# Kernel tuning notes

Measured on AMD Instinct MI355X. Metric: run time of the kernel, lower is better.

The kernel has to match this reference:

```python
import jax, jax.numpy as jnp
import numpy as np

EMBED, HIDDEN, VOCAB, FEAT_DIM = 256, 512, 10000, 1024
B, NREG, CAPLEN = 128, 49, 33


def setup_inputs() -> dict:
    key = jax.random.key(0)
    ks = jax.random.split(key, 20)
    xav = lambda k, shp: jax.random.uniform(k, shp, jnp.float32, -1.0, 1.0) * jnp.sqrt(6.0 / (shp[0] + shp[1]))
    d = {
        "features": jax.random.normal(ks[0], (B, NREG, FEAT_DIM), jnp.float32),
        "captions": jax.random.randint(ks[1], (B, CAPLEN), 0, VOCAB),
        "emb": jax.random.uniform(ks[2], (VOCAB, EMBED), jnp.float32, -0.1, 0.1),
        "W_ft": jax.random.uniform(ks[3], (EMBED, FEAT_DIM), jnp.float32, -0.1, 0.1),
        "b_ft": jnp.zeros((EMBED,), jnp.float32),
        "W_i": xav(ks[4], (2 * EMBED, HIDDEN)), "U_i": xav(ks[5], (HIDDEN, HIDDEN)), "b_i": jnp.zeros((HIDDEN,), jnp.float32),
        "W_f": xav(ks[6], (2 * EMBED, HIDDEN)), "U_f": xav(ks[7], (HIDDEN, HIDDEN)), "b_f": jnp.zeros((HIDDEN,), jnp.float32),
        "W_c": xav(ks[8], (2 * EMBED, HIDDEN)), "U_c": xav(ks[9], (HIDDEN, HIDDEN)), "b_c": jnp.zeros((HIDDEN,), jnp.float32),
        "W_o": xav(ks[10], (2 * EMBED, HIDDEN)), "U_o": xav(ks[11], (HIDDEN, HIDDEN)), "b_o": jnp.zeros((HIDDEN,), jnp.float32),
        "W_fc": jax.random.uniform(ks[12], (VOCAB, HIDDEN), jnp.float32, -0.1, 0.1),
        "b_fc": jnp.zeros((VOCAB,), jnp.float32),
    }
    return d


def reference(features, captions, emb, W_ft, b_ft,
              W_i, U_i, b_i, W_f, U_f, b_f, W_c, U_c, b_c, W_o, U_o, b_o,
              W_fc, b_fc):
    # mean-pool image regions, project to embed space
    feats_emb = features.mean(axis=1) @ W_ft.T + b_ft            # [B, E]
    embeds = emb[captions[:, :-1]]                                # [B, T, E]
    xs = jnp.swapaxes(embeds, 0, 1)                               # [T, B, E]

    h0 = jnp.zeros((features.shape[0], HIDDEN), features.dtype)
    c0 = jnp.zeros_like(h0)

    def step(carry, e_t):
        h, c = carry
        x = jnp.concatenate([e_t, feats_emb], axis=1)             # [B, 2E] (dropout=eval identity)
        i = jax.nn.sigmoid(x @ W_i + h @ U_i + b_i)
        f = jax.nn.sigmoid(x @ W_f + h @ U_f + b_f)
        g = jnp.tanh(x @ W_c + h @ U_c + b_c)
        o = jax.nn.sigmoid(x @ W_o + h @ U_o + b_o)
        c_new = f * c + i * g
        h_new = o * jnp.tanh(c_new)
        return (h_new, c_new), h_new

    _, hs = jax.lax.scan(step, (h0, c0), xs)                      # hs: [T, B, H]
    outputs = jnp.einsum('tbh,vh->btv', hs, W_fc) + b_fc          # [B, T, V]
    return outputs
```

## Files before the change

kernel.cpp:

```cpp
#include <hip/hip_runtime.h>
#include <hip/hip_bf16.h>

#define EMBED    256
#define HIDDEN   512
#define VOCAB    10000
#define FEAT_DIM 1024
#define BATCH    128
#define NREGS    49
#define TSTEPS   32

typedef unsigned short u16;
typedef unsigned long long u64;
using f32x4 = __attribute__((ext_vector_type(4))) float;
using s16x8 = __attribute__((ext_vector_type(8))) short;

__device__ __forceinline__ u16 f2bf(float f) {
  __hip_bfloat16 h = __float2bfloat16(f);
  return *reinterpret_cast<u16*>(&h);
}
__device__ __forceinline__ float sig_(float x) {
  return 1.0f / (1.0f + __expf(-x));
}
__device__ __forceinline__ float tanh_(float x) {
  x = fminf(fmaxf(x, -15.f), 15.f);
  float e = __expf(2.f * x);
  return (e - 1.f) / (e + 1.f);
}

__global__ __launch_bounds__(256)
void k_feats(const float* __restrict__ features, const float* __restrict__ W_ft,
             const float* __restrict__ b_ft, float* __restrict__ feats_emb) {
  __shared__ float mean[FEAT_DIM];
  int b = blockIdx.x, tid = threadIdx.x;
  const float* fb = features + (size_t)b * NREGS * FEAT_DIM;
  for (int d = tid; d < FEAT_DIM; d += 256) {
    float s = 0.f;
    for (int r = 0; r < NREGS; ++r) s += fb[r * FEAT_DIM + d];
    mean[d] = s * (1.0f / 49.0f);
  }
  __syncthreads();
  const float* w = W_ft + (size_t)tid * FEAT_DIM;
  float acc = b_ft[tid];
#pragma unroll 4
  for (int d = 0; d < FEAT_DIM; d += 4) {
    float4 m4 = *(const float4*)&mean[d];
    float4 w4 = *(const float4*)&w[d];
    acc += m4.x * w4.x + m4.y * w4.y + m4.z * w4.z + m4.w * w4.w;
  }
  feats_emb[b * EMBED + tid] = acc;
}

struct GatePtrs {
  const float* W[4];
  const float* U[4];
  const float* b[4];
};

__global__ __launch_bounds__(256)
void k_transpose_wu(GatePtrs p, u16* __restrict__ WcatT, u16* __restrict__ UcatT) {
  __shared__ float tile[64][65];
  int g = blockIdx.y;
  const float* src = blockIdx.z ? p.U[g] : p.W[g];
  u16* dst = blockIdx.z ? UcatT : WcatT;
  int tj = (blockIdx.x & 7) * 64;
  int tk = (blockIdx.x >> 3) * 64;
  int tx = threadIdx.x & 63, ty = threadIdx.x >> 6;
#pragma unroll
  for (int i = 0; i < 16; ++i)
    tile[ty + 4 * i][tx] = src[(size_t)(tk + ty + 4 * i) * HIDDEN + tj + tx];
  __syncthreads();
#pragma unroll
  for (int i = 0; i < 16; ++i)
    dst[(size_t)(g * 512 + tj + ty + 4 * i) * 512 + tk + tx] = f2bf(tile[tx][ty + 4 * i]);
}

__global__ __launch_bounds__(256)
void k_prep2(GatePtrs p, const float* __restrict__ W_fc,
             float* __restrict__ bcat, u16* __restrict__ Wfc_bf) {
  int idx = blockIdx.x * 256 + threadIdx.x;
  if (idx < VOCAB * HIDDEN / 4) {
    float4 v = *(const float4*)(W_fc + (size_t)idx * 4);
    ushort4 o;
    o.x = f2bf(v.x); o.y = f2bf(v.y); o.z = f2bf(v.z); o.w = f2bf(v.w);
    *(ushort4*)(Wfc_bf + (size_t)idx * 4) = o;
  }
  if (idx < 4 * HIDDEN) bcat[idx] = p.b[idx >> 9][idx & 511];
}

__global__ __launch_bounds__(256)
void k_build_x(const float* __restrict__ emb, const int* __restrict__ captions,
               const float* __restrict__ feats_emb, u16* __restrict__ X) {
  int idx = blockIdx.x * 256 + threadIdx.x;
  int r = idx >> 9, col = idx & 511;
  int t = r >> 7, b = r & 127;
  float v;
  if (col < EMBED) {
    int tok = captions[b * 33 + t];
    v = emb[(size_t)tok * EMBED + col];
  } else {
    v = feats_emb[b * EMBED + (col - EMBED)];
  }
  X[idx] = f2bf(v);
}

#define GSTR 40

__global__ __launch_bounds__(256)
void k_gemm_bt(const u16* __restrict__ A, const u16* __restrict__ Bt,
               const float* __restrict__ bias, float* __restrict__ C,
               int M, int N, int K, int out_mode) {
  __shared__ u16 Al[128 * GSTR];
  __shared__ u16 Bl[128 * GSTR];
  int tid = threadIdx.x;
  int lane = tid & 63;
  int w = tid >> 6;
  int wr = w & 1, wc = w >> 1;

  int Mtiles = gridDim.y, Ntiles = gridDim.x;
  int nwg = Mtiles * Ntiles;
  int id = blockIdx.y * Ntiles + blockIdx.x;
  int q = nwg >> 3, r = nwg & 7;
  int xcd = id & 7, pos = id >> 3;
  int wg = (xcd < r ? xcd * (q + 1) : r * (q + 1) + (xcd - r) * q) + pos;
  int m0 = (wg % Mtiles) * 128;
  int n0 = (wg / Mtiles) * 128;

  f32x4 acc[4][4];
#pragma unroll
  for (int i = 0; i < 4; ++i)
#pragma unroll
    for (int j = 0; j < 4; ++j) acc[i][j] = (f32x4){0.f, 0.f, 0.f, 0.f};

  int s0 = tid, s1 = tid + 256;
  int ar0 = s0 >> 2, ak0 = (s0 & 3) * 8;
  int ar1 = s1 >> 2, ak1 = (s1 & 3) * 8;

  for (int k0 = 0; k0 < K; k0 += 32) {
    uint4 a0 = *(const uint4*)(A + (size_t)(m0 + ar0) * K + k0 + ak0);
    uint4 a1 = *(const uint4*)(A + (size_t)(m0 + ar1) * K + k0 + ak1);
    uint4 b0, b1;
    int bn0 = n0 + ar0, bn1 = n0 + ar1;
    if (bn0 < N) b0 = *(const uint4*)(Bt + (size_t)bn0 * K + k0 + ak0);
    else { b0.x = b0.y = b0.z = b0.w = 0u; }
    if (bn1 < N) b1 = *(const uint4*)(Bt + (size_t)bn1 * K + k0 + ak1);
    else { b1.x = b1.y = b1.z = b1.w = 0u; }

    __syncthreads();
    *(uint4*)(Al + ar0 * GSTR + ak0) = a0;
    *(uint4*)(Al + ar1 * GSTR + ak1) = a1;
    *(uint4*)(Bl + ar0 * GSTR + ak0) = b0;
    *(uint4*)(Bl + ar1 * GSTR + ak1) = b1;
    __syncthreads();

    const u16* ab = Al + (wr * 64 + (lane & 15)) * GSTR + (lane >> 4) * 8;
    const u16* bb = Bl + (wc * 64 + (lane & 15)) * GSTR + (lane >> 4) * 8;
    s16x8 af[4], bf_[4];
#pragma unroll
    for (int mi = 0; mi < 4; ++mi) af[mi] = *(const s16x8*)(ab + mi * 16 * GSTR);
#pragma unroll
    for (int ni = 0; ni < 4; ++ni) bf_[ni] = *(const s16x8*)(bb + ni * 16 * GSTR);
#pragma unroll
    for (int mi = 0; mi < 4; ++mi)
#pragma unroll
      for (int ni = 0; ni < 4; ++ni)
        acc[mi][ni] = __builtin_amdgcn_mfma_f32_16x16x32_bf16(af[mi], bf_[ni], acc[mi][ni], 0, 0, 0);
  }

  int rbase = (lane >> 4) * 4;
  int colf = lane & 15;
#pragma unroll
  for (int mi = 0; mi < 4; ++mi) {
    int mbase = m0 + wr * 64 + mi * 16 + rbase;
#pragma unroll
    for (int ni = 0; ni < 4; ++ni) {
      int n = n0 + wc * 64 + ni * 16 + colf;
      if (n < N) {
        float bv = bias[n];
#pragma unroll
        for (int reg = 0; reg < 4; ++reg) {
          int mm = mbase + reg;
          float v = acc[mi][ni][reg] + bv;
          if (out_mode == 0) {
            C[(size_t)mm * N + n] = v;
          } else {
            C[(size_t)(mm & 127) * (TSTEPS * VOCAB) + (size_t)(mm >> 7) * VOCAB + n] = v;
          }
        }
      }
    }
  }
}

#define USTR 520

__global__ __launch_bounds__(256, 1)
void k_lstm_all(const u16* __restrict__ UcatT, const float* __restrict__ gates_pre,
                u16* __restrict__ hs, unsigned* __restrict__ hx, int* __restrict__ bar) {
  __shared__ u16 Ul[128 * USTR];
  int tid = threadIdx.x;
  int lane = tid & 63;
  int w = tid >> 6;
  int wr = w & 1, wj = w >> 1;
  int mg = blockIdx.x >> 4;
  int jb = blockIdx.x & 15;
  int b0 = mg * 32;
  int j0 = jb * 32;

  for (int i = tid; i < 128 * 64; i += 256) {
    int row = i >> 6;
    int kc = (i & 63) * 8;
    int gr = ((row >> 5) << 9) + j0 + (row & 31);
    uint4 v = *(const uint4*)(UcatT + (size_t)gr * 512 + kc);
    *(uint4*)(Ul + row * USTR + kc) = v;
  }
  __syncthreads();

  int jloc = wj * 16 + (lane & 15);
  int jj = j0 + jloc;
  int rb = wr * 16 + (lane >> 4) * 4;
  int arow = b0 + wr * 16 + (lane & 15);
  const u16* ubase = Ul + (size_t)jloc * USTR + (lane >> 4) * 8;
  const u64* hx64 = (const u64*)hx;
  int* flag = bar + mg * 64;

  float c[4] = {0.f, 0.f, 0.f, 0.f};
  float gpv[16];

#pragma unroll
  for (int reg = 0; reg < 4; ++reg)
#pragma unroll
    for (int gi = 0; gi < 4; ++gi)
      gpv[reg * 4 + gi] = gates_pre[((size_t)(b0 + rb + reg)) * 2048 + gi * 512 + jj];

#pragma unroll 1
  for (int t = 0; t < TSTEPS; ++t) {
    f32x4 acc[4];
#pragma unroll
    for (int gi = 0; gi < 4; ++gi) acc[gi] = (f32x4){0.f, 0.f, 0.f, 0.f};

    if (t > 0) {
      const u64* hrow = hx64 + ((size_t)(t - 1) * 128 + arow) * 128 + (lane >> 4) * 2;
      s16x8 af[16];
#pragma unroll
      for (int kk = 0; kk < 16; ++kk) {
        u64 q0 = __hip_atomic_load(hrow + kk * 8,     __ATOMIC_RELAXED, __HIP_MEMORY_SCOPE_AGENT);
        u64 q1 = __hip_atomic_load(hrow + kk * 8 + 1, __ATOMIC_RELAXED, __HIP_MEMORY_SCOPE_AGENT);
        union { u64 q[2]; s16x8 v; } u;
        u.q[0] = q0; u.q[1] = q1;
        af[kk] = u.v;
      }
#pragma unroll
      for (int kk = 0; kk < 16; ++kk) {
#pragma unroll
        for (int gi = 0; gi < 4; ++gi) {
          s16x8 bf_ = *(const s16x8*)(ubase + (size_t)gi * 32 * USTR + kk * 32);
          acc[gi] = __builtin_amdgcn_mfma_f32_16x16x32_bf16(af[kk], bf_, acc[gi], 0, 0, 0);
        }
      }
    }

#pragma unroll
    for (int reg = 0; reg < 4; ++reg) {
      float pi = acc[0][reg] + gpv[reg * 4 + 0];
      float pf = acc[1][reg] + gpv[reg * 4 + 1];
      float pg = acc[2][reg] + gpv[reg * 4 + 2];
      float po = acc[3][reg] + gpv[reg * 4 + 3];
      float iv = sig_(pi), fv = sig_(pf), gv = tanh_(pg), ov = sig_(po);
      float cn = fv * c[reg] + iv * gv;
      c[reg] = cn;
      float hn = ov * tanh_(cn);
      u16 hb = f2bf(hn);
      hs[((size_t)t * 128 + b0 + rb + reg) * 512 + jj] = hb;
      unsigned pv = hb;
      unsigned nv = __shfl_down(pv, 1);
      if ((lane & 1) == 0) {
        unsigned packed = pv | (nv << 16);
        __hip_atomic_store(hx + ((size_t)t * 128 + b0 + rb + reg) * 256 + (jj >> 1),
                           packed, __ATOMIC_RELAXED, __HIP_MEMORY_SCOPE_AGENT);
      }
    }

    if (t < TSTEPS - 1) {
#pragma unroll
      for (int reg = 0; reg < 4; ++reg)
#pragma unroll
        for (int gi = 0; gi < 4; ++gi)
          gpv[reg * 4 + gi] =
              gates_pre[((size_t)(t + 1) * 128 + b0 + rb + reg) * 2048 + gi * 512 + jj];

      __syncthreads();
      if (tid == 0) {
        __hip_atomic_fetch_add(flag, 1, __ATOMIC_RELAXED, __HIP_MEMORY_SCOPE_AGENT);
        int target = 16 * (t + 1);
        while (__hip_atomic_load(flag, __ATOMIC_RELAXED, __HIP_MEMORY_SCOPE_AGENT) < target) {}
      }
      __syncthreads();
    }
  }
}

extern "C" void kernel_launch(void* const* d_in, const int* in_sizes, int n_in,
                              void* d_out, int out_size, void* d_ws, size_t ws_size,
                              hipStream_t stream) {
  const float* features = (const float*)d_in[0];
  const int*   captions = (const int*)d_in[1];
  const float* emb      = (const float*)d_in[2];
  const float* W_ft     = (const float*)d_in[3];
  const float* b_ft     = (const float*)d_in[4];
  GatePtrs p;
  p.W[0] = (const float*)d_in[5];  p.U[0] = (const float*)d_in[6];  p.b[0] = (const float*)d_in[7];
  p.W[1] = (const float*)d_in[8];  p.U[1] = (const float*)d_in[9];  p.b[1] = (const float*)d_in[10];
  p.W[2] = (const float*)d_in[11]; p.U[2] = (const float*)d_in[12]; p.b[2] = (const float*)d_in[13];
  p.W[3] = (const float*)d_in[14]; p.U[3] = (const float*)d_in[15]; p.b[3] = (const float*)d_in[16];
  const float* W_fc = (const float*)d_in[17];
  const float* b_fc = (const float*)d_in[18];
  float* out = (float*)d_out;

  char* ws = (char*)d_ws;
  float*    feats_emb = (float*)(ws + 0);
  u16*      X         = (u16*)(ws + 131072);
  unsigned* hx        = (unsigned*)(ws + 131072);
  u16*      WcatT     = (u16*)(ws + 4325376);
  u16*      UcatT     = (u16*)(ws + 6422528);
  float*    bcat      = (float*)(ws + 8519680);
  u16*      Wfc_bf    = (u16*)(ws + 8527872);
  float*    gates_pre = (float*)(ws + 18767872);
  int*      bar       = (int*)(ws + 52322304);
  u16*      hs        = (u16*)(ws + 52846592);

  hipMemsetAsync(bar, 0, 4 * 64 * sizeof(int), stream);

  k_feats<<<128, 256, 0, stream>>>(features, W_ft, b_ft, feats_emb);
  k_transpose_wu<<<dim3(64, 4, 2), 256, 0, stream>>>(p, WcatT, UcatT);
  k_prep2<<<(VOCAB * HIDDEN / 4 + 255) / 256, 256, 0, stream>>>(p, W_fc, bcat, Wfc_bf);
  k_build_x<<<(TSTEPS * BATCH * 2 * EMBED) / 256, 256, 0, stream>>>(emb, captions, feats_emb, X);

  k_gemm_bt<<<dim3(2048 / 128, 4096 / 128), 256, 0, stream>>>(
      X, WcatT, bcat, gates_pre, 4096, 2048, 512, 0);

  k_lstm_all<<<64, 256, 0, stream>>>(UcatT, gates_pre, hs, hx, bar);

  k_gemm_bt<<<dim3((VOCAB + 127) / 128, 4096 / 128), 256, 0, stream>>>(
      hs, Wfc_bf, b_fc, out, 4096, VOCAB, 512, 1);
}
```

Baseline: 371.0 us.

## Replace LSTM step barrier with sentinel-polled hidden state and drop duplicate hs store

The recurrent kernel no longer uses a per-group atomic counter barrier with two __syncthreads per step. The hidden-state buffer is pre-filled with a 0xFFFFFFFF sentinel, and each wave re-polls only the words that still hold the sentinel until producer blocks have written them. The same buffer then serves directly as the bf16 hs input to the vocab GEMM, which removes the separate hs store. This relies on a bf16 pair never encoding 0xFFFF/0xFFFF (NaN) and adds a memset of the 4 MB buffer.

Result: slower. 446.3 us (+20.3%).

```diff
diff --git a/kernel.cpp b/kernel.cpp
--- a/kernel.cpp
+++ b/kernel.cpp
@@ -192,10 +192,11 @@
 }
 
 #define USTR 520
+#define SENT 0xFFFFFFFFu
 
 __global__ __launch_bounds__(256, 1)
 void k_lstm_all(const u16* __restrict__ UcatT, const float* __restrict__ gates_pre,
-                u16* __restrict__ hs, unsigned* __restrict__ hx, int* __restrict__ bar) {
+                unsigned* __restrict__ hx) {
   __shared__ u16 Ul[128 * USTR];
   int tid = threadIdx.x;
   int lane = tid & 63;
@@ -221,7 +222,6 @@
   int arow = b0 + wr * 16 + (lane & 15);
   const u16* ubase = Ul + (size_t)jloc * USTR + (lane >> 4) * 8;
   const u64* hx64 = (const u64*)hx;
-  int* flag = bar + mg * 64;
 
   float c[4] = {0.f, 0.f, 0.f, 0.f};
   float gpv[16];
@@ -240,21 +240,35 @@
 
     if (t > 0) {
       const u64* hrow = hx64 + ((size_t)(t - 1) * 128 + arow) * 128 + (lane >> 4) * 2;
-      s16x8 af[16];
+      union Frag { u64 q[2]; unsigned u[4]; s16x8 v; };
+      Frag fr[16];
 #pragma unroll
       for (int kk = 0; kk < 16; ++kk) {
-        u64 q0 = __hip_atomic_load(hrow + kk * 8,     __ATOMIC_RELAXED, __HIP_MEMORY_SCOPE_AGENT);
-        u64 q1 = __hip_atomic_load(hrow + kk * 8 + 1, __ATOMIC_RELAXED, __HIP_MEMORY_SCOPE_AGENT);
-        union { u64 q[2]; s16x8 v; } u;
-        u.q[0] = q0; u.q[1] = q1;
-        af[kk] = u.v;
+        fr[kk].q[0] = __hip_atomic_load(hrow + kk * 8,     __ATOMIC_RELAXED, __HIP_MEMORY_SCOPE_AGENT);
+        fr[kk].q[1] = __hip_atomic_load(hrow + kk * 8 + 1, __ATOMIC_RELAXED, __HIP_MEMORY_SCOPE_AGENT);
       }
+      bool ok;
+      do {
+        ok = true;
+#pragma unroll
+        for (int kk = 0; kk < 16; ++kk) {
+#pragma unroll
+          for (int h = 0; h < 2; ++h) {
+            if (fr[kk].u[2 * h] == SENT || fr[kk].u[2 * h + 1] == SENT) {
+              fr[kk].q[h] = __hip_atomic_load(hrow + kk * 8 + h,
+                                              __ATOMIC_RELAXED, __HIP_MEMORY_SCOPE_AGENT);
+              ok = false;
+            }
+          }
+        }
+      } while (__builtin_expect(!ok, 0));
+
 #pragma unroll
       for (int kk = 0; kk < 16; ++kk) {
 #pragma unroll
         for (int gi = 0; gi < 4; ++gi) {
           s16x8 bf_ = *(const s16x8*)(ubase + (size_t)gi * 32 * USTR + kk * 32);
-          acc[gi] = __builtin_amdgcn_mfma_f32_16x16x32_bf16(af[kk], bf_, acc[gi], 0, 0, 0);
+          acc[gi] = __builtin_amdgcn_mfma_f32_16x16x32_bf16(fr[kk].v, bf_, acc[gi], 0, 0, 0);
         }
       }
     }
@@ -270,7 +284,6 @@
       c[reg] = cn;
       float hn = ov * tanh_(cn);
       u16 hb = f2bf(hn);
-      hs[((size_t)t * 128 + b0 + rb + reg) * 512 + jj] = hb;
       unsigned pv = hb;
       unsigned nv = __shfl_down(pv, 1);
       if ((lane & 1) == 0) {
@@ -287,14 +300,6 @@
         for (int gi = 0; gi < 4; ++gi)
           gpv[reg * 4 + gi] =
               gates_pre[((size_t)(t + 1) * 128 + b0 + rb + reg) * 2048 + gi * 512 + jj];
-
-      __syncthreads();
-      if (tid == 0) {
-        __hip_atomic_fetch_add(flag, 1, __ATOMIC_RELAXED, __HIP_MEMORY_SCOPE_AGENT);
-        int target = 16 * (t + 1);
-        while (__hip_atomic_load(flag, __ATOMIC_RELAXED, __HIP_MEMORY_SCOPE_AGENT) < target) {}
-      }
-      __syncthreads();
     }
   }
 }
@@ -319,16 +324,14 @@
   char* ws = (char*)d_ws;
   float*    feats_emb = (float*)(ws + 0);
   u16*      X         = (u16*)(ws + 131072);
-  unsigned* hx        = (unsigned*)(ws + 131072);
   u16*      WcatT     = (u16*)(ws + 4325376);
   u16*      UcatT     = (u16*)(ws + 6422528);
   float*    bcat      = (float*)(ws + 8519680);
   u16*      Wfc_bf    = (u16*)(ws + 8527872);
   float*    gates_pre = (float*)(ws + 18767872);
-  int*      bar       = (int*)(ws + 52322304);
-  u16*      hs        = (u16*)(ws + 52846592);
-
-  hipMemsetAsync(bar, 0, 4 * 64 * sizeof(int), stream);
+  unsigned* hx        = (unsigned*)(ws + 52846592);
+
+  hipMemsetAsync(hx, 0xFF, (size_t)TSTEPS * BATCH * HIDDEN * 2, stream);
 
   k_feats<<<128, 256, 0, stream>>>(features, W_ft, b_ft, feats_emb);
   k_transpose_wu<<<dim3(64, 4, 2), 256, 0, stream>>>(p, WcatT, UcatT);
@@ -338,8 +341,8 @@
   k_gemm_bt<<<dim3(2048 / 128, 4096 / 128), 256, 0, stream>>>(
       X, WcatT, bcat, gates_pre, 4096, 2048, 512, 0);
 
-  k_lstm_all<<<64, 256, 0, stream>>>(UcatT, gates_pre, hs, hx, bar);
+  k_lstm_all<<<64, 256, 0, stream>>>(UcatT, gates_pre, hx);
 
   k_gemm_bt<<<dim3((VOCAB + 127) / 128, 4096 / 128), 256, 0, stream>>>(
-      hs, Wfc_bf, b_fc, out, 4096, VOCAB, 512, 1);
-}
+      (const u16*)hx, Wfc_bf, b_fc, out, 4096, VOCAB, 512, 1);
+}
```

## Use direct global-to-LDS loads in GEMM and per-block flags for LSTM sync

Applied to the files above, without the earlier changes.

The GEMM now stages A and B tiles with global_load_lds into unpadded shared memory, skipping the register round trip. To drop the N bounds check, W_fc is zero-padded to a multiple of 128 rows. The LSTM replaces its shared atomic counter barrier with per-block monotonic flags that consumers poll only when they need h. It also drops the duplicate hs store and feeds hx straight into the output GEMM. Risks are LDS bank conflicts from the unpadded stride and the weaker ordering of relaxed flag stores.

New measurement: 375.0 us. Within noise of the previous version (+1.1%).

```diff
diff --git a/kernel.cpp b/kernel.cpp
--- a/kernel.cpp
+++ b/kernel.cpp
@@ -4,6 +4,7 @@
 #define EMBED    256
 #define HIDDEN   512
 #define VOCAB    10000
+#define WFC_PAD  10112
 #define FEAT_DIM 1024
 #define BATCH    128
 #define NREGS    49
@@ -25,6 +26,11 @@
   x = fminf(fmaxf(x, -15.f), 15.f);
   float e = __expf(2.f * x);
   return (e - 1.f) / (e + 1.f);
+}
+__device__ __forceinline__ void gl_lds16(const u16* g, u16* l) {
+  __builtin_amdgcn_global_load_lds(
+      (const __attribute__((address_space(1))) unsigned*)g,
+      (__attribute__((address_space(3))) unsigned*)l, 16, 0, 0);
 }
 
 __global__ __launch_bounds__(256)
@@ -78,11 +84,16 @@
 void k_prep2(GatePtrs p, const float* __restrict__ W_fc,
              float* __restrict__ bcat, u16* __restrict__ Wfc_bf) {
   int idx = blockIdx.x * 256 + threadIdx.x;
-  if (idx < VOCAB * HIDDEN / 4) {
-    float4 v = *(const float4*)(W_fc + (size_t)idx * 4);
+  if (idx < WFC_PAD * HIDDEN / 4) {
+    size_t e0 = (size_t)idx * 4;
     ushort4 o;
-    o.x = f2bf(v.x); o.y = f2bf(v.y); o.z = f2bf(v.z); o.w = f2bf(v.w);
-    *(ushort4*)(Wfc_bf + (size_t)idx * 4) = o;
+    if (e0 < (size_t)VOCAB * HIDDEN) {
+      float4 v = *(const float4*)(W_fc + e0);
+      o.x = f2bf(v.x); o.y = f2bf(v.y); o.z = f2bf(v.z); o.w = f2bf(v.w);
+    } else {
+      o.x = o.y = o.z = o.w = 0;
+    }
+    *(ushort4*)(Wfc_bf + e0) = o;
   }
   if (idx < 4 * HIDDEN) bcat[idx] = p.b[idx >> 9][idx & 511];
 }
@@ -103,14 +114,12 @@
   X[idx] = f2bf(v);
 }
 
-#define GSTR 40
-
 __global__ __launch_bounds__(256)
 void k_gemm_bt(const u16* __restrict__ A, const u16* __restrict__ Bt,
                const float* __restrict__ bias, float* __restrict__ C,
                int M, int N, int K, int out_mode) {
-  __shared__ u16 Al[128 * GSTR];
-  __shared__ u16 Bl[128 * GSTR];
+  __shared__ u16 Al[128 * 32];
+  __shared__ u16 Bl[128 * 32];
   int tid = threadIdx.x;
   int lane = tid & 63;
   int w = tid >> 6;
@@ -131,34 +140,26 @@
 #pragma unroll
     for (int j = 0; j < 4; ++j) acc[i][j] = (f32x4){0.f, 0.f, 0.f, 0.f};
 
-  int s0 = tid, s1 = tid + 256;
-  int ar0 = s0 >> 2, ak0 = (s0 & 3) * 8;
-  int ar1 = s1 >> 2, ak1 = (s1 & 3) * 8;
+  int srowq = lane >> 2;
+  int skq   = (lane & 3) * 8;
 
   for (int k0 = 0; k0 < K; k0 += 32) {
-    uint4 a0 = *(const uint4*)(A + (size_t)(m0 + ar0) * K + k0 + ak0);
-    uint4 a1 = *(const uint4*)(A + (size_t)(m0 + ar1) * K + k0 + ak1);
-    uint4 b0, b1;
-    int bn0 = n0 + ar0, bn1 = n0 + ar1;
-    if (bn0 < N) b0 = *(const uint4*)(Bt + (size_t)bn0 * K + k0 + ak0);
-    else { b0.x = b0.y = b0.z = b0.w = 0u; }
-    if (bn1 < N) b1 = *(const uint4*)(Bt + (size_t)bn1 * K + k0 + ak1);
-    else { b1.x = b1.y = b1.z = b1.w = 0u; }
-
     __syncthreads();
-    *(uint4*)(Al + ar0 * GSTR + ak0) = a0;
-    *(uint4*)(Al + ar1 * GSTR + ak1) = a1;
-    *(uint4*)(Bl + ar0 * GSTR + ak0) = b0;
-    *(uint4*)(Bl + ar1 * GSTR + ak1) = b1;
+#pragma unroll
+    for (int i = 0; i < 2; ++i) {
+      int rr = w * 32 + i * 16;
+      gl_lds16(A + (size_t)(m0 + rr + srowq) * K + k0 + skq, Al + rr * 32);
+      gl_lds16(Bt + (size_t)(n0 + rr + srowq) * K + k0 + skq, Bl + rr * 32);
+    }
     __syncthreads();
 
-    const u16* ab = Al + (wr * 64 + (lane & 15)) * GSTR + (lane >> 4) * 8;
-    const u16* bb = Bl + (wc * 64 + (lane & 15)) * GSTR + (lane >> 4) * 8;
+    const u16* ab = Al + (wr * 64 + (lane & 15)) * 32 + (lane >> 4) * 8;
+    const u16* bb = Bl + (wc * 64 + (lane & 15)) * 32 + (lane >> 4) * 8;
     s16x8 af[4], bf_[4];
 #pragma unroll
-    for (int mi = 0; mi < 4; ++mi) af[mi] = *(const s16x8*)(ab + mi * 16 * GSTR);
-#pragma unroll
-    for (int ni = 0; ni < 4; ++ni) bf_[ni] = *(const s16x8*)(bb + ni * 16 * GSTR);
+    for (int mi = 0; mi < 4; ++mi) af[mi] = *(const s16x8*)(ab + mi * 16 * 32);
+#pragma unroll
+    for (int ni = 0; ni < 4; ++ni) bf_[ni] = *(const s16x8*)(bb + ni * 16 * 32);
 #pragma unroll
     for (int mi = 0; mi < 4; ++mi)
 #pragma unroll
@@ -195,7 +196,7 @@
 
 __global__ __launch_bounds__(256, 1)
 void k_lstm_all(const u16* __restrict__ UcatT, const float* __restrict__ gates_pre,
-                u16* __restrict__ hs, unsigned* __restrict__ hx, int* __restrict__ bar) {
+                unsigned* __restrict__ hx, int* __restrict__ flags) {
   __shared__ u16 Ul[128 * USTR];
   int tid = threadIdx.x;
   int lane = tid & 63;
@@ -221,7 +222,8 @@
   int arow = b0 + wr * 16 + (lane & 15);
   const u16* ubase = Ul + (size_t)jloc * USTR + (lane >> 4) * 8;
   const u64* hx64 = (const u64*)hx;
-  int* flag = bar + mg * 64;
+  int* myflag = flags + (mg * 16 + jb) * 16;
+  int* pollp  = flags + (mg * 16 + (lane & 15)) * 16;
 
   float c[4] = {0.f, 0.f, 0.f, 0.f};
   float gpv[16];
@@ -239,6 +241,11 @@
     for (int gi = 0; gi < 4; ++gi) acc[gi] = (f32x4){0.f, 0.f, 0.f, 0.f};
 
     if (t > 0) {
+      while (true) {
+        int fv = __hip_atomic_load(pollp, __ATOMIC_RELAXED, __HIP_MEMORY_SCOPE_AGENT);
+        if (__all((lane < 16) ? (fv >= t) : 1)) break;
+      }
+
       const u64* hrow = hx64 + ((size_t)(t - 1) * 128 + arow) * 128 + (lane >> 4) * 2;
       s16x8 af[16];
 #pragma unroll
@@ -270,7 +277,6 @@
       c[reg] = cn;
       float hn = ov * tanh_(cn);
       u16 hb = f2bf(hn);
-      hs[((size_t)t * 128 + b0 + rb + reg) * 512 + jj] = hb;
       unsigned pv = hb;
       unsigned nv = __shfl_down(pv, 1);
       if ((lane & 1) == 0) {
@@ -289,12 +295,8 @@
               gates_pre[((size_t)(t + 1) * 128 + b0 + rb + reg) * 2048 + gi * 512 + jj];
 
       __syncthreads();
-      if (tid == 0) {
-        __hip_atomic_fetch_add(flag, 1, __ATOMIC_RELAXED, __HIP_MEMORY_SCOPE_AGENT);
-        int target = 16 * (t + 1);
-        while (__hip_atomic_load(flag, __ATOMIC_RELAXED, __HIP_MEMORY_SCOPE_AGENT) < target) {}
-      }
-      __syncthreads();
+      if (tid == 0)
+        __hip_atomic_store(myflag, t + 1, __ATOMIC_RELAXED, __HIP_MEMORY_SCOPE_AGENT);
     }
   }
 }
@@ -319,27 +321,26 @@
   char* ws = (char*)d_ws;
   float*    feats_emb = (float*)(ws + 0);
   u16*      X         = (u16*)(ws + 131072);
-  unsigned* hx        = (unsigned*)(ws + 131072);
   u16*      WcatT     = (u16*)(ws + 4325376);
   u16*      UcatT     = (u16*)(ws + 6422528);
   float*    bcat      = (float*)(ws + 8519680);
   u16*      Wfc_bf    = (u16*)(ws + 8527872);
-  float*    gates_pre = (float*)(ws + 18767872);
-  int*      bar       = (int*)(ws + 52322304);
-  u16*      hs        = (u16*)(ws + 52846592);
-
-  hipMemsetAsync(bar, 0, 4 * 64 * sizeof(int), stream);
+  float*    gates_pre = (float*)(ws + 18882560);
+  int*      flags     = (int*)(ws + 52436992);
+  unsigned* hx        = (unsigned*)(ws + 52846592);
+
+  hipMemsetAsync(flags, 0, 64 * 64, stream);
 
   k_feats<<<128, 256, 0, stream>>>(features, W_ft, b_ft, feats_emb);
   k_transpose_wu<<<dim3(64, 4, 2), 256, 0, stream>>>(p, WcatT, UcatT);
-  k_prep2<<<(VOCAB * HIDDEN / 4 + 255) / 256, 256, 0, stream>>>(p, W_fc, bcat, Wfc_bf);
+  k_prep2<<<(WFC_PAD * HIDDEN / 4 + 255) / 256, 256, 0, stream>>>(p, W_fc, bcat, Wfc_bf);
   k_build_x<<<(TSTEPS * BATCH * 2 * EMBED) / 256, 256, 0, stream>>>(emb, captions, feats_emb, X);
 
   k_gemm_bt<<<dim3(2048 / 128, 4096 / 128), 256, 0, stream>>>(
       X, WcatT, bcat, gates_pre, 4096, 2048, 512, 0);
 
-  k_lstm_all<<<64, 256, 0, stream>>>(UcatT, gates_pre, hs, hx, bar);
-
-  k_gemm_bt<<<dim3((VOCAB + 127) / 128, 4096 / 128), 256, 0, stream>>>(
-      hs, Wfc_bf, b_fc, out, 4096, VOCAB, 512, 1);
-}
+  k_lstm_all<<<64, 256, 0, stream>>>(UcatT, gates_pre, hx, flags);
+
+  k_gemm_bt<<<dim3(WFC_PAD / 128, 4096 / 128), 256, 0, stream>>>(
+      (const u16*)hx, Wfc_bf, b_fc, out, 4096, VOCAB, 512, 1);
+}
```
